# Kernel tuning notes

Measured on AMD Instinct MI355X. Metric: run time of the kernel, lower is better.

The kernel has to match this reference:

```python
import jax, jax.numpy as jnp
import numpy as np
from jax import lax

T_STEPS = 1024
BATCH = 1024
NUM_STATES = 64


def setup_inputs() -> dict:
    key = jax.random.key(0)
    k_em, k_len, k_start, k_stop, k_trans = jax.random.split(key, 5)
    emission_factors = jax.random.normal(k_em, (T_STEPS, BATCH, NUM_STATES), dtype=jnp.float32)
    sequence_sizes = jax.random.randint(k_len, (BATCH,), 1, T_STEPS + 1, dtype=jnp.int32)
    start_factors = jax.random.normal(k_start, (NUM_STATES,), dtype=jnp.float32)
    stop_factors = jax.random.normal(k_stop, (NUM_STATES,), dtype=jnp.float32)
    transition_factors = jax.random.normal(k_trans, (NUM_STATES, NUM_STATES), dtype=jnp.float32)
    return {
        "emission_factors": emission_factors,
        "sequence_sizes": sequence_sizes,
        "start_factors": start_factors,
        "stop_factors": stop_factors,
        "transition_factors": transition_factors,
    }


def reference(emission_factors, sequence_sizes, start_factors, stop_factors, transition_factors):
    # emission_factors: [T, B, S] time-major; sequence_sizes: [B] lengths in [1, T].
    # Linear-chain CRF forward algorithm (log-partition):
    #   alpha_0   = start + em_0
    #   alpha_t[s] = logsumexp_p(alpha_{t-1}[p] + trans[s, p]) + em_t[s]   (while active)
    #   log_Z     = logsumexp_s(alpha_{L-1}[s] + stop[s])
    # Masked scan: alpha is frozen once a sequence ends, matching the packed
    # variable-batch-size iteration of the original (penultimate_alphas).
    max_steps = emission_factors.shape[0]

    alpha0 = start_factors[None, :] + emission_factors[0]  # [B, S]
    # active[t-1, b] = (t < length_b) for t = 1..T-1
    active = (jnp.arange(1, max_steps)[:, None] < sequence_sizes[None, :])[:, :, None]  # [T-1, B, 1]

    def step(alpha, inp):
        em_t, act = inp  # em_t: [B, S], act: [B, 1]
        # alpha[b, None, p] + trans[None, s, p] -> logsumexp over p
        new_alpha = jax.nn.logsumexp(alpha[:, None, :] + transition_factors[None, :, :], axis=2) + em_t
        return jnp.where(act, new_alpha, alpha), None

    alpha, _ = lax.scan(step, alpha0, (emission_factors[1:], active))
    log_normalizer = jax.nn.logsumexp(alpha + stop_factors[None, :], axis=1)  # [B]
    return log_normalizer
```

## Files before the change

kernel.cpp:

```cpp
#include <hip/hip_runtime.h>

#define T_STEPS 1024
#define BATCH   1024
#define NS      64

__global__ __launch_bounds__(64)
__attribute__((amdgpu_waves_per_eu(1, 1)))
void crf_fwd_readlane(const float* __restrict__ em,
                      const int*   __restrict__ seqlen,
                      const float* __restrict__ start,
                      const float* __restrict__ stop,
                      const float* __restrict__ trans,
                      float*       __restrict__ out) {
    const int b = blockIdx.x;
    const int s = threadIdx.x;
    const int L = seqlen[b];
    const int total = L - 1;

    float e[NS];
    {
        const float4* t4 = reinterpret_cast<const float4*>(trans + s * NS);
        #pragma unroll
        for (int i = 0; i < NS / 4; ++i) {
            float4 t = t4[i];
            e[4 * i + 0] = __expf(t.x);
            e[4 * i + 1] = __expf(t.y);
            e[4 * i + 2] = __expf(t.z);
            e[4 * i + 3] = __expf(t.w);
        }
    }
    #pragma unroll
    for (int i = 0; i < NS; ++i) asm volatile("" : "+v"(e[i]));

    float u = __expf(start[s] + em[(size_t)b * NS + s]);
    float c = 0.f;

    const float*  gp      = em + (size_t)b * NS + s;
    const size_t  TSTRIDE = (size_t)BATCH * NS;

    auto step = [&](float em_t) {
        unsigned ui = __float_as_uint(u) + 0x8000u;
        unsigned pi = __builtin_amdgcn_mov_dpp(ui, 0xB1, 0xF, 0xF, true);
        unsigned pk = __builtin_amdgcn_perm(pi, ui, 0x07060302u);
        float a0 = 0.f, a1 = 0.f, a2 = 0.f, a3 = 0.f;
        #pragma unroll
        for (int k = 0; k < 16; ++k) {
            const unsigned p0 = __builtin_amdgcn_readlane(pk, 4 * k);
            const unsigned p1 = __builtin_amdgcn_readlane(pk, 4 * k + 2);
            a0 = fmaf(e[4 * k + 0], __uint_as_float(p0 << 16),        a0);
            a1 = fmaf(e[4 * k + 1], __uint_as_float(p0 & 0xFFFF0000u), a1);
            a2 = fmaf(e[4 * k + 2], __uint_as_float(p1 << 16),        a2);
            a3 = fmaf(e[4 * k + 3], __uint_as_float(p1 & 0xFFFF0000u), a3);
        }
        u = ((a0 + a1) + (a2 + a3)) * __expf(em_t);
    };

    auto renorm = [&]() {
        float m = __uint_as_float(__builtin_amdgcn_readlane(__float_as_uint(u), 0));
        m = fmaxf(m, 1e-30f);
        u *= __builtin_amdgcn_rcpf(m);
        c += __logf(m);
    };

    float emq[4];
    #pragma unroll
    for (int j = 0; j < 4; ++j) {
        int t = 1 + j; if (t > T_STEPS - 1) t = T_STEPS - 1;
        emq[j] = gp[(size_t)t * TSTRIDE];
    }

    int done = 0;
    while (done + 4 <= total) {
        float emn[4];
        #pragma unroll
        for (int j = 0; j < 4; ++j) {
            int t = done + 5 + j; if (t > T_STEPS - 1) t = T_STEPS - 1;
            emn[j] = gp[(size_t)t * TSTRIDE];
        }

        renorm();
        step(emq[0]); step(emq[1]); step(emq[2]); step(emq[3]);

        #pragma unroll
        for (int j = 0; j < 4; ++j) emq[j] = emn[j];
        done += 4;
    }

    const int tail = total - done;
    if (tail > 0) {
        renorm();
        for (int j = 0; j < tail; ++j) step(emq[j]);
    }

    float v = u * __expf(stop[s]);
    #pragma unroll
    for (int o = 1; o < 64; o <<= 1) v += __shfl_xor(v, o, 64);
    if (s == 0) out[b] = __logf(v) + c;
}

extern "C" void kernel_launch(void* const* d_in, const int* in_sizes, int n_in,
                              void* d_out, int out_size, void* d_ws, size_t ws_size,
                              hipStream_t stream) {
    const float* em     = (const float*)d_in[0];
    const int*   seqlen = (const int*)  d_in[1];
    const float* start  = (const float*)d_in[2];
    const float* stop   = (const float*)d_in[3];
    const float* trans  = (const float*)d_in[4];
    float*       out    = (float*)d_out;

    crf_fwd_readlane<<<BATCH, NS, 0, stream>>>(em, seqlen, start, stop, trans, out);
}
```

Baseline: 634.8 us.

## Use full-precision readlane broadcasts, fold renorm into emission, prefetch eight steps

Replaces the bf16-packed DPP/perm broadcast (two values per readlane) with 64 plain fp32 readlanes per step, issued in two batches of 32 separated by a sched_barrier so the scalar reads can pipeline ahead of the FMAs. Renormalization is folded into the emission multiplier instead of a separate pass over u. Emission exps are computed ahead of the dependent chain, and the prefetch depth grows from 4 to 8 steps. This removes the packing work and restores precision, but doubles the number of readlane instructions on the serial critical path and increases register pressure.

Result: faster. 524.5 us (-17.4%).

```diff
diff --git a/kernel.cpp b/kernel.cpp
--- a/kernel.cpp
+++ b/kernel.cpp
@@ -6,12 +6,12 @@
 
 __global__ __launch_bounds__(64)
 __attribute__((amdgpu_waves_per_eu(1, 1)))
-void crf_fwd_readlane(const float* __restrict__ em,
-                      const int*   __restrict__ seqlen,
-                      const float* __restrict__ start,
-                      const float* __restrict__ stop,
-                      const float* __restrict__ trans,
-                      float*       __restrict__ out) {
+void crf_fwd_v4(const float* __restrict__ em,
+                const int*   __restrict__ seqlen,
+                const float* __restrict__ start,
+                const float* __restrict__ stop,
+                const float* __restrict__ trans,
+                float*       __restrict__ out) {
     const int b = blockIdx.x;
     const int s = threadIdx.x;
     const int L = seqlen[b];
@@ -34,63 +34,66 @@
 
     float u = __expf(start[s] + em[(size_t)b * NS + s]);
     float c = 0.f;
+    const float*  gp = em + (size_t)b * NS + s;
+    const size_t  TS = (size_t)BATCH * NS;
 
-    const float*  gp      = em + (size_t)b * NS + s;
-    const size_t  TSTRIDE = (size_t)BATCH * NS;
-
-    auto step = [&](float em_t) {
-        unsigned ui = __float_as_uint(u) + 0x8000u;
-        unsigned pi = __builtin_amdgcn_mov_dpp(ui, 0xB1, 0xF, 0xF, true);
-        unsigned pk = __builtin_amdgcn_perm(pi, ui, 0x07060302u);
+    auto step = [&](float ex, bool rn) {
+        const unsigned ub = __float_as_uint(u);
+        if (rn) {
+            float m = __uint_as_float(__builtin_amdgcn_readlane(ub, 0));
+            m = fmaxf(m, 1e-30f);
+            ex *= __builtin_amdgcn_rcpf(m);
+            c += __logf(m);
+        }
         float a0 = 0.f, a1 = 0.f, a2 = 0.f, a3 = 0.f;
         #pragma unroll
-        for (int k = 0; k < 16; ++k) {
-            const unsigned p0 = __builtin_amdgcn_readlane(pk, 4 * k);
-            const unsigned p1 = __builtin_amdgcn_readlane(pk, 4 * k + 2);
-            a0 = fmaf(e[4 * k + 0], __uint_as_float(p0 << 16),        a0);
-            a1 = fmaf(e[4 * k + 1], __uint_as_float(p0 & 0xFFFF0000u), a1);
-            a2 = fmaf(e[4 * k + 2], __uint_as_float(p1 << 16),        a2);
-            a3 = fmaf(e[4 * k + 3], __uint_as_float(p1 & 0xFFFF0000u), a3);
+        for (int h = 0; h < 2; ++h) {
+            unsigned g[32];
+            #pragma unroll
+            for (int j = 0; j < 32; ++j)
+                g[j] = __builtin_amdgcn_readlane(ub, 32 * h + j);
+            __builtin_amdgcn_sched_barrier(0);
+            #pragma unroll
+            for (int j = 0; j < 8; ++j) {
+                a0 = fmaf(e[32 * h + 4 * j + 0], __uint_as_float(g[4 * j + 0]), a0);
+                a1 = fmaf(e[32 * h + 4 * j + 1], __uint_as_float(g[4 * j + 1]), a1);
+                a2 = fmaf(e[32 * h + 4 * j + 2], __uint_as_float(g[4 * j + 2]), a2);
+                a3 = fmaf(e[32 * h + 4 * j + 3], __uint_as_float(g[4 * j + 3]), a3);
+            }
         }
-        u = ((a0 + a1) + (a2 + a3)) * __expf(em_t);
+        u = ((a0 + a1) + (a2 + a3)) * ex;
     };
 
-    auto renorm = [&]() {
-        float m = __uint_as_float(__builtin_amdgcn_readlane(__float_as_uint(u), 0));
-        m = fmaxf(m, 1e-30f);
-        u *= __builtin_amdgcn_rcpf(m);
-        c += __logf(m);
-    };
-
-    float emq[4];
+    float emq[8];
     #pragma unroll
-    for (int j = 0; j < 4; ++j) {
+    for (int j = 0; j < 8; ++j) {
         int t = 1 + j; if (t > T_STEPS - 1) t = T_STEPS - 1;
-        emq[j] = gp[(size_t)t * TSTRIDE];
+        emq[j] = gp[(size_t)t * TS];
     }
 
     int done = 0;
-    while (done + 4 <= total) {
-        float emn[4];
+    while (done + 8 <= total) {
+        float emn[8];
         #pragma unroll
-        for (int j = 0; j < 4; ++j) {
-            int t = done + 5 + j; if (t > T_STEPS - 1) t = T_STEPS - 1;
-            emn[j] = gp[(size_t)t * TSTRIDE];
+        for (int j = 0; j < 8; ++j) {
+            int t = done + 9 + j; if (t > T_STEPS - 1) t = T_STEPS - 1;
+            emn[j] = gp[(size_t)t * TS];
         }
+        float ex[8];
+        #pragma unroll
+        for (int j = 0; j < 8; ++j) ex[j] = __expf(emq[j]);
 
-        renorm();
-        step(emq[0]); step(emq[1]); step(emq[2]); step(emq[3]);
+        step(ex[0], true);  step(ex[1], false); step(ex[2], false); step(ex[3], false);
+        step(ex[4], true);  step(ex[5], false); step(ex[6], false); step(ex[7], false);
 
         #pragma unroll
-        for (int j = 0; j < 4; ++j) emq[j] = emn[j];
-        done += 4;
+        for (int j = 0; j < 8; ++j) emq[j] = emn[j];
+        done += 8;
     }
 
     const int tail = total - done;
-    if (tail > 0) {
-        renorm();
-        for (int j = 0; j < tail; ++j) step(emq[j]);
-    }
+    for (int j = 0; j < tail; ++j)
+        step(__expf(emq[j]), (j & 3) == 0);
 
     float v = u * __expf(stop[s]);
     #pragma unroll
@@ -108,5 +111,5 @@
     const float* trans  = (const float*)d_in[4];
     float*       out    = (float*)d_out;
 
-    crf_fwd_readlane<<<BATCH, NS, 0, stream>>>(em, seqlen, start, stop, trans, out);
+    crf_fwd_v4<<<BATCH, NS, 0, stream>>>(em, seqlen, start, stop, trans, out);
 }
```
